# Optimization experiments

Measured on AMD Instinct MI355X. Metric: run time of the kernel, lower is better.

Reference implementation:

```python
import jax, jax.numpy as jnp
import numpy as np

LN_EPS = 1e-5

def layernorm(x, w, b):
    mu = jnp.mean(x, axis=-1, keepdims=True)
    var = jnp.mean(jnp.square(x - mu), axis=-1, keepdims=True)
    return (x - mu) * jax.lax.rsqrt(var + LN_EPS) * w + b

def l2_normalize(x, eps=1e-12):
    n = jnp.sqrt(jnp.sum(jnp.square(x), axis=-1, keepdims=True))
    return x / jnp.maximum(n, eps)

def setup_inputs() -> dict:
    key = jax.random.key(0)
    k1, k2 = jax.random.split(key)
    B, D, Npix = 8, 64, 32768
    K, P = 19, 5
    return {
        "base_feature": jax.random.normal(k1, (B, D, Npix), dtype=jnp.float32),
        "means": jax.random.normal(k2, (K, P, D), dtype=jnp.float32) * 0.02,  # trunc_normal_(std=0.02)
        "diagonal": jnp.ones((K, P, D), dtype=jnp.float32),
        "feat_w": jnp.ones((D,), dtype=jnp.float32),
        "feat_b": jnp.zeros((D,), dtype=jnp.float32),
        "mask_w": jnp.ones((K,), dtype=jnp.float32),
        "mask_b": jnp.zeros((K,), dtype=jnp.float32),
    }

def gmm_log_prob(x, mu, scale):
    # x: [N, D]; mu, scale: [KP, D]  (MultivariateNormalDiag with scale_diag=scale)
    # log p = -0.5 * sum(((x-mu)/s)^2) - sum(log s) - 0.5*D*log(2*pi)
    D = x.shape[-1]
    inv2 = 1.0 / jnp.square(scale)                      # [KP, D]
    quad = (jnp.square(x) @ inv2.T                       # [N, KP]
            - 2.0 * (x @ (mu * inv2).T)
            + jnp.sum(jnp.square(mu) * inv2, axis=-1))
    log_norm = jnp.sum(jnp.log(scale), axis=-1) + 0.5 * D * jnp.log(2.0 * jnp.pi)
    return -0.5 * quad - log_norm                        # [N, KP]

def reference(base_feature, means, diagonal, feat_w, feat_b, mask_w, mask_b):
    B, D, Npix = base_feature.shape
    K, P, _ = means.shape
    # 'b c n -> (b n) c'
    _c = jnp.transpose(base_feature, (0, 2, 1)).reshape(B * Npix, D)
    _c = layernorm(_c, feat_w, feat_b)
    _c = l2_normalize(_c)
    means_n = l2_normalize(means)                        # means.data.copy_(l2_normalize(means))
    logp = gmm_log_prob(_c, means_n.reshape(K * P, D), diagonal.reshape(K * P, D))
    final_probs = logp.reshape(-1, K, P)                 # [(b n), K, P]
    _m_prob = jnp.max(final_probs, axis=-1)              # amax over components -> [(b n), K]
    out_seg = layernorm(_m_prob, mask_w, mask_b)         # mask_norm
    # '(b n) k -> b k n'
    out_seg = jnp.transpose(out_seg.reshape(B, Npix, K), (0, 2, 1))
    return out_seg
```

## Files before the change

kernel.cpp:

```cpp
#include <hip/hip_runtime.h>
#include <math.h>

#define BB    8
#define DD    64
#define NPIX  32768
#define KK    19
#define PP    5
#define KP    95
#define KPAD  96

typedef _Float16 half8  __attribute__((ext_vector_type(8)));
typedef __fp16   half2t __attribute__((ext_vector_type(2)));
typedef float    f32x4  __attribute__((ext_vector_type(4)));

union H8 { half8 v; half2t p[4]; };

__global__ __launch_bounds__(64) void gmm_prep(
        const float* __restrict__ means, const float* __restrict__ diag,
        const float* __restrict__ feat_w, const float* __restrict__ feat_b,
        _Float16* __restrict__ Ch, float* __restrict__ cst,
        float* __restrict__ scal) {
    int j = blockIdx.x;
    int d = threadIdx.x;
    if (j < KP) {
        float mu = means[j * DD + d];
        float sc = diag[j * DD + d];
        float ss = mu * mu;
        #pragma unroll
        for (int off = 32; off; off >>= 1) ss += __shfl_xor(ss, off);
        float inv = 1.f / fmaxf(sqrtf(ss), 1e-12f);
        float mn = mu * inv;
        float i2 = 1.f / (sc * sc);
        Ch[j * 128 + 2 * d]     = (_Float16)(mn * i2);
        Ch[j * 128 + 2 * d + 1] = (_Float16)(-0.5f * i2);
        float c1 = mn * mn * i2;
        float c2 = logf(sc);
        #pragma unroll
        for (int off = 32; off; off >>= 1) {
            c1 += __shfl_xor(c1, off);
            c2 += __shfl_xor(c2, off);
        }
        if (d == 0) cst[j] = -0.5f * c1 - c2 - 58.8120661251f;
    } else {
        Ch[95 * 128 + 2 * d]     = (_Float16)0.f;
        Ch[95 * 128 + 2 * d + 1] = (_Float16)0.f;
        float w = feat_w[d], b = feat_b[d];
        float s0 = w * w, s1 = w * b, s2 = b * b;
        #pragma unroll
        for (int off = 32; off; off >>= 1) {
            s0 += __shfl_xor(s0, off);
            s1 += __shfl_xor(s1, off);
            s2 += __shfl_xor(s2, off);
        }
        if (d == 0) { cst[95] = 0.f; scal[0] = s0; scal[1] = s1; scal[2] = s2; }
    }
}

#define LPS 98

__global__ __launch_bounds__(256, 2) void gmm_main(
        const float* __restrict__ bf,
        const float* __restrict__ feat_w, const float* __restrict__ feat_b,
        const float* __restrict__ mask_w, const float* __restrict__ mask_b,
        const _Float16* __restrict__ Ch, const float* __restrict__ cst,
        const float* __restrict__ scal, float* __restrict__ out) {
    __shared__ float lds[4][32 * LPS];

    const int tid  = threadIdx.x;
    const int w    = tid >> 6;
    const int lane = tid & 63;
    const int m15  = lane & 15;
    const int q    = lane >> 4;
    const int bidx = blockIdx.x;
    const int b    = bidx >> 8;
    const int n0   = ((bidx & 255) << 7) + (w << 5);
    float* lp = lds[w];

    const float* xp = bf + (size_t)b * (DD * NPIX) + n0 + m15;
    float xs0[16], xs1[16];
    #pragma unroll
    for (int ks = 0; ks < 4; ++ks)
        #pragma unroll
        for (int i = 0; i < 4; ++i) {
            const size_t off = (size_t)(ks * 16 + q * 4 + i) * NPIX;
            xs0[ks * 4 + i] = xp[off];
            xs1[ks * 4 + i] = xp[off + 16];
        }

    float4 wv[4], bv[4];
    #pragma unroll
    for (int ks = 0; ks < 4; ++ks) {
        wv[ks] = *(const float4*)(feat_w + ks * 16 + q * 4);
        bv[ks] = *(const float4*)(feat_b + ks * 16 + q * 4);
    }

    float S1a = 0.f, S2a = 0.f, S3a = 0.f, S4a = 0.f, S5a = 0.f;
    float S1b = 0.f, S2b = 0.f, S3b = 0.f, S4b = 0.f, S5b = 0.f;
    #pragma unroll
    for (int ks = 0; ks < 4; ++ks)
        #pragma unroll
        for (int i = 0; i < 4; ++i) {
            float wd = ((const float*)&wv[ks])[i];
            float bd = ((const float*)&bv[ks])[i];
            float xa = xs0[ks * 4 + i], xb = xs1[ks * 4 + i];
            float ta = wd * xa, tb = wd * xb;
            S1a += xa; S2a = fmaf(xa, xa, S2a); S3a = fmaf(ta, ta, S3a);
            S4a = fmaf(ta, wd, S4a); S5a = fmaf(ta, bd, S5a);
            S1b += xb; S2b = fmaf(xb, xb, S2b); S3b = fmaf(tb, tb, S3b);
            S4b = fmaf(tb, wd, S4b); S5b = fmaf(tb, bd, S5b);
        }
    S1a += __shfl_xor(S1a, 16); S1a += __shfl_xor(S1a, 32);
    S2a += __shfl_xor(S2a, 16); S2a += __shfl_xor(S2a, 32);
    S3a += __shfl_xor(S3a, 16); S3a += __shfl_xor(S3a, 32);
    S4a += __shfl_xor(S4a, 16); S4a += __shfl_xor(S4a, 32);
    S5a += __shfl_xor(S5a, 16); S5a += __shfl_xor(S5a, 32);
    S1b += __shfl_xor(S1b, 16); S1b += __shfl_xor(S1b, 32);
    S2b += __shfl_xor(S2b, 16); S2b += __shfl_xor(S2b, 32);
    S3b += __shfl_xor(S3b, 16); S3b += __shfl_xor(S3b, 32);
    S4b += __shfl_xor(S4b, 16); S4b += __shfl_xor(S4b, 32);
    S5b += __shfl_xor(S5b, 16); S5b += __shfl_xor(S5b, 32);

    const float W2 = scal[0], WB = scal[1], B2 = scal[2];
    float al0, e0, f0, al1, e1, f1;
    {
        float mu  = S1a * (1.f / 64.f);
        float var = fmaxf(S2a * (1.f / 64.f) - mu * mu, 0.f);
        float r   = rsqrtf(var + 1e-5f);
        float Sy2 = r * r * (S3a - 2.f * mu * S4a + mu * mu * W2)
                  + 2.f * r * (S5a - mu * WB) + B2;
        float invn = 1.f / fmaxf(sqrtf(fmaxf(Sy2, 0.f)), 1e-12f);
        al0 = invn * r; e0 = invn; f0 = -al0 * mu;
    }
    {
        float mu  = S1b * (1.f / 64.f);
        float var = fmaxf(S2b * (1.f / 64.f) - mu * mu, 0.f);
        float r   = rsqrtf(var + 1e-5f);
        float Sy2 = r * r * (S3b - 2.f * mu * S4b + mu * mu * W2)
                  + 2.f * r * (S5b - mu * WB) + B2;
        float invn = 1.f / fmaxf(sqrtf(fmaxf(Sy2, 0.f)), 1e-12f);
        al1 = invn * r; e1 = invn; f1 = -al1 * mu;
    }

    H8 Uh[2][4], Ul[2][4];
    #pragma unroll
    for (int ks = 0; ks < 4; ++ks) {
        #pragma unroll
        for (int i = 0; i < 4; ++i) {
            float wd = ((const float*)&wv[ks])[i];
            float bd = ((const float*)&bv[ks])[i];
            float c0 = fmaf(f0, wd, e0 * bd);
            float c1 = fmaf(f1, wd, e1 * bd);
            float u0 = fmaf(al0, wd * xs0[ks * 4 + i], c0);
            float u1 = fmaf(al1, wd * xs1[ks * 4 + i], c1);
            float q0 = u0 * u0, q1 = u1 * u1;
            half2t h0 = __builtin_amdgcn_cvt_pkrtz(u0, q0);
            half2t h1 = __builtin_amdgcn_cvt_pkrtz(u1, q1);
            half2t l0 = __builtin_amdgcn_cvt_pkrtz(u0 - (float)h0[0], q0 - (float)h0[1]);
            half2t l1 = __builtin_amdgcn_cvt_pkrtz(u1 - (float)h1[0], q1 - (float)h1[1]);
            Uh[0][ks].p[i] = h0; Ul[0][ks].p[i] = l0;
            Uh[1][ks].p[i] = h1; Ul[1][ks].p[i] = l1;
        }
    }

    const _Float16* cb = Ch + (size_t)m15 * 128 + q * 8;
    half8 Ac[4];
    #pragma unroll
    for (int ks = 0; ks < 4; ++ks) Ac[ks] = *(const half8*)(cb + ks * 32);
    float4 cc = *(const float4*)(cst + 4 * q);

    #pragma unroll 2
    for (int t = 0; t < 6; ++t) {
        half8 An[4];
        float4 cn;
        if (t < 5) {
            const _Float16* nb = cb + (size_t)(16 * (t + 1)) * 128;
            #pragma unroll
            for (int ks = 0; ks < 4; ++ks) An[ks] = *(const half8*)(nb + ks * 32);
            cn = *(const float4*)(cst + 16 * (t + 1) + 4 * q);
        }
        f32x4 a0 = {0.f, 0.f, 0.f, 0.f}, a1 = a0;
        #pragma unroll
        for (int ks = 0; ks < 4; ++ks) {
            a0 = __builtin_amdgcn_mfma_f32_16x16x32_f16(Ac[ks], Uh[0][ks].v, a0, 0, 0, 0);
            a1 = __builtin_amdgcn_mfma_f32_16x16x32_f16(Ac[ks], Uh[1][ks].v, a1, 0, 0, 0);
        }
        #pragma unroll
        for (int ks = 0; ks < 4; ++ks) {
            a0 = __builtin_amdgcn_mfma_f32_16x16x32_f16(Ac[ks], Ul[0][ks].v, a0, 0, 0, 0);
            a1 = __builtin_amdgcn_mfma_f32_16x16x32_f16(Ac[ks], Ul[1][ks].v, a1, 0, 0, 0);
        }
        {
            const int j0 = 16 * t + 4 * q;
            float2 v00 = make_float2(a0[0] + cc[0], a0[1] + cc[1]);
            float2 v01 = make_float2(a0[2] + cc[2], a0[3] + cc[3]);
            float2 v10 = make_float2(a1[0] + cc[0], a1[1] + cc[1]);
            float2 v11 = make_float2(a1[2] + cc[2], a1[3] + cc[3]);
            *(float2*)(lp + m15 * LPS + j0)            = v00;
            *(float2*)(lp + m15 * LPS + j0 + 2)        = v01;
            *(float2*)(lp + (16 + m15) * LPS + j0)     = v10;
            *(float2*)(lp + (16 + m15) * LPS + j0 + 2) = v11;
        }
        if (t < 5) {
            #pragma unroll
            for (int ks = 0; ks < 4; ++ks) Ac[ks] = An[ks];
            cc = cn;
        }
    }

    const int px2 = lane & 31;
    const int h   = lane >> 5;
    const int kb  = h ? 9 : 0;
    const int ke  = h ? 19 : 9;
    const float* rowp = lp + px2 * LPS;
    float mv[10];
    float S = 0.f;
    #pragma unroll
    for (int kk = 0; kk < 10; ++kk) {
        const int k = kb + kk;
        float best = -3.4e38f;
        if (k < ke) {
            #pragma unroll
            for (int p = 0; p < PP; ++p)
                best = fmaxf(best, rowp[5 * k + p]);
            S += best;
        }
        mv[kk] = best;
    }
    S += __shfl_xor(S, 32);
    const float mum = S * (1.f / 19.f);
    float V = 0.f;
    #pragma unroll
    for (int kk = 0; kk < 10; ++kk) {
        if (kb + kk < ke) { float t = mv[kk] - mum; V = fmaf(t, t, V); }
    }
    V += __shfl_xor(V, 32);
    const float rm = rsqrtf(V * (1.f / 19.f) + 1e-5f);

    float* op = out + (size_t)b * (KK * NPIX) + n0 + px2;
    #pragma unroll
    for (int kk = 0; kk < 10; ++kk) {
        const int k = kb + kk;
        if (k < ke)
            op[(size_t)k * NPIX] = (mv[kk] - mum) * rm * mask_w[k] + mask_b[k];
    }
}

extern "C" void kernel_launch(void* const* d_in, const int* in_sizes, int n_in,
                              void* d_out, int out_size, void* d_ws, size_t ws_size,
                              hipStream_t stream) {
    const float* base_feature = (const float*)d_in[0];
    const float* means        = (const float*)d_in[1];
    const float* diagonal     = (const float*)d_in[2];
    const float* feat_w       = (const float*)d_in[3];
    const float* feat_b       = (const float*)d_in[4];
    const float* mask_w       = (const float*)d_in[5];
    const float* mask_b       = (const float*)d_in[6];
    float* out = (float*)d_out;

    _Float16* Ch = (_Float16*)d_ws;
    float* cst   = (float*)(Ch + KPAD * 128);
    float* scal  = cst + KPAD;

    gmm_prep<<<KPAD, 64, 0, stream>>>(means, diagonal, feat_w, feat_b, Ch, cst, scal);

    gmm_main<<<(BB * NPIX) / 128, 256, 0, stream>>>(
        base_feature, feat_w, feat_b, mask_w, mask_b, Ch, cst, scal, out);
}
```

Baseline: 137.9 us.

## Permute GMM component rows so max and mask-norm stay in MFMA registers

The prep kernel reorders the component rows (padded to 112) so that each MFMA output lane holds the same component index for a fixed cluster across tiles. The max over components, the mask layernorm and the output then run directly on accumulator registers with cross-lane shuffles, which removes the LDS staging buffer and the shared-memory round trip. Dropping the LDS lets the launch bounds rise to 4 blocks per SM, but the kernel now runs 7 MFMA tiles instead of 6, which is extra padded compute. The constant log-normalisation term is dropped because the final layernorm cancels it.

Result: slower. 140.8 us (+2.1%).

```diff
diff --git a/kernel.cpp b/kernel.cpp
--- a/kernel.cpp
+++ b/kernel.cpp
@@ -6,8 +6,7 @@
 #define NPIX  32768
 #define KK    19
 #define PP    5
-#define KP    95
-#define KPAD  96
+#define NROW  112
 
 typedef _Float16 half8  __attribute__((ext_vector_type(8)));
 typedef __fp16   half2t __attribute__((ext_vector_type(2)));
@@ -20,9 +19,26 @@
         const float* __restrict__ feat_w, const float* __restrict__ feat_b,
         _Float16* __restrict__ Ch, float* __restrict__ cst,
         float* __restrict__ scal) {
-    int j = blockIdx.x;
-    int d = threadIdx.x;
-    if (j < KP) {
+    const int R = blockIdx.x;
+    const int d = threadIdx.x;
+    if (R == NROW) {
+        float w = feat_w[d], b = feat_b[d];
+        float s0 = w * w, s1 = w * b, s2 = b * b;
+        #pragma unroll
+        for (int off = 32; off; off >>= 1) {
+            s0 += __shfl_xor(s0, off);
+            s1 += __shfl_xor(s1, off);
+            s2 += __shfl_xor(s2, off);
+        }
+        if (d == 0) { scal[0] = s0; scal[1] = s1; scal[2] = s2; }
+        return;
+    }
+    int g, p; bool valid;
+    if (R < 80)      { g = 4 * (R >> 4) + ((R >> 2) & 3); p = R & 3; valid = (g < KK); }
+    else if (R < 96) { g = 4 * ((R - 80) & 3) + ((R - 80) >> 2); p = 4; valid = true; }
+    else             { g = 16 + ((R - 96) >> 2); p = 4; valid = ((R & 3) == 0) && (g < KK); }
+    if (valid) {
+        const int j = 5 * g + p;
         float mu = means[j * DD + d];
         float sc = diag[j * DD + d];
         float ss = mu * mu;
@@ -31,8 +47,8 @@
         float inv = 1.f / fmaxf(sqrtf(ss), 1e-12f);
         float mn = mu * inv;
         float i2 = 1.f / (sc * sc);
-        Ch[j * 128 + 2 * d]     = (_Float16)(mn * i2);
-        Ch[j * 128 + 2 * d + 1] = (_Float16)(-0.5f * i2);
+        Ch[R * 128 + 2 * d]     = (_Float16)(mn * i2);
+        Ch[R * 128 + 2 * d + 1] = (_Float16)(-0.5f * i2);
         float c1 = mn * mn * i2;
         float c2 = logf(sc);
         #pragma unroll
@@ -40,32 +56,65 @@
             c1 += __shfl_xor(c1, off);
             c2 += __shfl_xor(c2, off);
         }
-        if (d == 0) cst[j] = -0.5f * c1 - c2 - 58.8120661251f;
+        if (d == 0) cst[R] = -0.5f * c1 - c2;
     } else {
-        Ch[95 * 128 + 2 * d]     = (_Float16)0.f;
-        Ch[95 * 128 + 2 * d + 1] = (_Float16)0.f;
-        float w = feat_w[d], b = feat_b[d];
-        float s0 = w * w, s1 = w * b, s2 = b * b;
-        #pragma unroll
-        for (int off = 32; off; off >>= 1) {
-            s0 += __shfl_xor(s0, off);
-            s1 += __shfl_xor(s1, off);
-            s2 += __shfl_xor(s2, off);
-        }
-        if (d == 0) { cst[95] = 0.f; scal[0] = s0; scal[1] = s1; scal[2] = s2; }
-    }
-}
-
-#define LPS 98
-
-__global__ __launch_bounds__(256, 2) void gmm_main(
+        Ch[R * 128 + 2 * d]     = (_Float16)0.f;
+        Ch[R * 128 + 2 * d + 1] = (_Float16)0.f;
+        if (d == 0) cst[R] = 0.f;
+    }
+}
+
+#define DO_TILE(T, MERGE) {                                                   \
+    const _Float16* ab = cb + (size_t)((T) * 16 * 128);                       \
+    const half8 A0 = *(const half8*)(ab);                                     \
+    const half8 A1 = *(const half8*)(ab + 32);                                \
+    const half8 A2 = *(const half8*)(ab + 64);                                \
+    const half8 A3 = *(const half8*)(ab + 96);                                \
+    const float4 cc = *(const float4*)(cst + 16 * (T) + 4 * q);               \
+    f32x4 a0 = {0.f, 0.f, 0.f, 0.f}, a1 = {0.f, 0.f, 0.f, 0.f};               \
+    a0 = __builtin_amdgcn_mfma_f32_16x16x32_f16(A0, Uh[0][0].v, a0, 0, 0, 0); \
+    a1 = __builtin_amdgcn_mfma_f32_16x16x32_f16(A0, Uh[1][0].v, a1, 0, 0, 0); \
+    a0 = __builtin_amdgcn_mfma_f32_16x16x32_f16(A1, Uh[0][1].v, a0, 0, 0, 0); \
+    a1 = __builtin_amdgcn_mfma_f32_16x16x32_f16(A1, Uh[1][1].v, a1, 0, 0, 0); \
+    a0 = __builtin_amdgcn_mfma_f32_16x16x32_f16(A2, Uh[0][2].v, a0, 0, 0, 0); \
+    a1 = __builtin_amdgcn_mfma_f32_16x16x32_f16(A2, Uh[1][2].v, a1, 0, 0, 0); \
+    a0 = __builtin_amdgcn_mfma_f32_16x16x32_f16(A3, Uh[0][3].v, a0, 0, 0, 0); \
+    a1 = __builtin_amdgcn_mfma_f32_16x16x32_f16(A3, Uh[1][3].v, a1, 0, 0, 0); \
+    a0 = __builtin_amdgcn_mfma_f32_16x16x32_f16(A0, Ul[0][0].v, a0, 0, 0, 0); \
+    a1 = __builtin_amdgcn_mfma_f32_16x16x32_f16(A0, Ul[1][0].v, a1, 0, 0, 0); \
+    a0 = __builtin_amdgcn_mfma_f32_16x16x32_f16(A1, Ul[0][1].v, a0, 0, 0, 0); \
+    a1 = __builtin_amdgcn_mfma_f32_16x16x32_f16(A1, Ul[1][1].v, a1, 0, 0, 0); \
+    a0 = __builtin_amdgcn_mfma_f32_16x16x32_f16(A2, Ul[0][2].v, a0, 0, 0, 0); \
+    a1 = __builtin_amdgcn_mfma_f32_16x16x32_f16(A2, Ul[1][2].v, a1, 0, 0, 0); \
+    a0 = __builtin_amdgcn_mfma_f32_16x16x32_f16(A3, Ul[0][3].v, a0, 0, 0, 0); \
+    a1 = __builtin_amdgcn_mfma_f32_16x16x32_f16(A3, Ul[1][3].v, a1, 0, 0, 0); \
+    MERGE                                                                     \
+}
+
+#define MERGE_SLOT(T)                                                              \
+    m0[T] = fmaxf(fmaxf(a0[0] + cc.x, a0[1] + cc.y), fmaxf(a0[2] + cc.z, a0[3] + cc.w)); \
+    m1[T] = fmaxf(fmaxf(a1[0] + cc.x, a1[1] + cc.y), fmaxf(a1[2] + cc.z, a1[3] + cc.w));
+
+#define MERGE_C4A                                                \
+    m0[0] = fmaxf(m0[0], a0[0] + cc.x);                          \
+    m0[1] = fmaxf(m0[1], a0[1] + cc.y);                          \
+    m0[2] = fmaxf(m0[2], a0[2] + cc.z);                          \
+    m0[3] = fmaxf(m0[3], a0[3] + cc.w);                          \
+    m1[0] = fmaxf(m1[0], a1[0] + cc.x);                          \
+    m1[1] = fmaxf(m1[1], a1[1] + cc.y);                          \
+    m1[2] = fmaxf(m1[2], a1[2] + cc.z);                          \
+    m1[3] = fmaxf(m1[3], a1[3] + cc.w);
+
+#define MERGE_C4B                                                \
+    m0[4] = fmaxf(m0[4], a0[0] + cc.x);                          \
+    m1[4] = fmaxf(m1[4], a1[0] + cc.x);
+
+__global__ __launch_bounds__(256, 4) void gmm_main(
         const float* __restrict__ bf,
         const float* __restrict__ feat_w, const float* __restrict__ feat_b,
         const float* __restrict__ mask_w, const float* __restrict__ mask_b,
         const _Float16* __restrict__ Ch, const float* __restrict__ cst,
         const float* __restrict__ scal, float* __restrict__ out) {
-    __shared__ float lds[4][32 * LPS];
-
     const int tid  = threadIdx.x;
     const int w    = tid >> 6;
     const int lane = tid & 63;
@@ -74,7 +123,6 @@
     const int bidx = blockIdx.x;
     const int b    = bidx >> 8;
     const int n0   = ((bidx & 255) << 7) + (w << 5);
-    float* lp = lds[w];
 
     const float* xp = bf + (size_t)b * (DD * NPIX) + n0 + m15;
     float xs0[16], xs1[16];
@@ -163,85 +211,46 @@
     }
 
     const _Float16* cb = Ch + (size_t)m15 * 128 + q * 8;
-    half8 Ac[4];
-    #pragma unroll
-    for (int ks = 0; ks < 4; ++ks) Ac[ks] = *(const half8*)(cb + ks * 32);
-    float4 cc = *(const float4*)(cst + 4 * q);
-
-    #pragma unroll 2
-    for (int t = 0; t < 6; ++t) {
-        half8 An[4];
-        float4 cn;
-        if (t < 5) {
-            const _Float16* nb = cb + (size_t)(16 * (t + 1)) * 128;
-            #pragma unroll
-            for (int ks = 0; ks < 4; ++ks) An[ks] = *(const half8*)(nb + ks * 32);
-            cn = *(const float4*)(cst + 16 * (t + 1) + 4 * q);
-        }
-        f32x4 a0 = {0.f, 0.f, 0.f, 0.f}, a1 = a0;
-        #pragma unroll
-        for (int ks = 0; ks < 4; ++ks) {
-            a0 = __builtin_amdgcn_mfma_f32_16x16x32_f16(Ac[ks], Uh[0][ks].v, a0, 0, 0, 0);
-            a1 = __builtin_amdgcn_mfma_f32_16x16x32_f16(Ac[ks], Uh[1][ks].v, a1, 0, 0, 0);
-        }
-        #pragma unroll
-        for (int ks = 0; ks < 4; ++ks) {
-            a0 = __builtin_amdgcn_mfma_f32_16x16x32_f16(Ac[ks], Ul[0][ks].v, a0, 0, 0, 0);
-            a1 = __builtin_amdgcn_mfma_f32_16x16x32_f16(Ac[ks], Ul[1][ks].v, a1, 0, 0, 0);
-        }
-        {
-            const int j0 = 16 * t + 4 * q;
-            float2 v00 = make_float2(a0[0] + cc[0], a0[1] + cc[1]);
-            float2 v01 = make_float2(a0[2] + cc[2], a0[3] + cc[3]);
-            float2 v10 = make_float2(a1[0] + cc[0], a1[1] + cc[1]);
-            float2 v11 = make_float2(a1[2] + cc[2], a1[3] + cc[3]);
-            *(float2*)(lp + m15 * LPS + j0)            = v00;
-            *(float2*)(lp + m15 * LPS + j0 + 2)        = v01;
-            *(float2*)(lp + (16 + m15) * LPS + j0)     = v10;
-            *(float2*)(lp + (16 + m15) * LPS + j0 + 2) = v11;
-        }
-        if (t < 5) {
-            #pragma unroll
-            for (int ks = 0; ks < 4; ++ks) Ac[ks] = An[ks];
-            cc = cn;
-        }
-    }
-
-    const int px2 = lane & 31;
-    const int h   = lane >> 5;
-    const int kb  = h ? 9 : 0;
-    const int ke  = h ? 19 : 9;
-    const float* rowp = lp + px2 * LPS;
-    float mv[10];
-    float S = 0.f;
-    #pragma unroll
-    for (int kk = 0; kk < 10; ++kk) {
-        const int k = kb + kk;
-        float best = -3.4e38f;
-        if (k < ke) {
-            #pragma unroll
-            for (int p = 0; p < PP; ++p)
-                best = fmaxf(best, rowp[5 * k + p]);
-            S += best;
-        }
-        mv[kk] = best;
-    }
-    S += __shfl_xor(S, 32);
-    const float mum = S * (1.f / 19.f);
-    float V = 0.f;
-    #pragma unroll
-    for (int kk = 0; kk < 10; ++kk) {
-        if (kb + kk < ke) { float t = mv[kk] - mum; V = fmaf(t, t, V); }
-    }
-    V += __shfl_xor(V, 32);
-    const float rm = rsqrtf(V * (1.f / 19.f) + 1e-5f);
-
-    float* op = out + (size_t)b * (KK * NPIX) + n0 + px2;
-    #pragma unroll
-    for (int kk = 0; kk < 10; ++kk) {
-        const int k = kb + kk;
-        if (k < ke)
-            op[(size_t)k * NPIX] = (mv[kk] - mum) * rm * mask_w[k] + mask_b[k];
+    float m0[5], m1[5];
+    DO_TILE(0, MERGE_SLOT(0))
+    DO_TILE(1, MERGE_SLOT(1))
+    DO_TILE(2, MERGE_SLOT(2))
+    DO_TILE(3, MERGE_SLOT(3))
+    DO_TILE(4, MERGE_SLOT(4))
+    DO_TILE(5, MERGE_C4A)
+    DO_TILE(6, MERGE_C4B)
+
+    const bool v4 = (q < 3);
+    float S0 = m0[0] + m0[1] + m0[2] + m0[3] + (v4 ? m0[4] : 0.f);
+    float S1 = m1[0] + m1[1] + m1[2] + m1[3] + (v4 ? m1[4] : 0.f);
+    S0 += __shfl_xor(S0, 16); S0 += __shfl_xor(S0, 32);
+    S1 += __shfl_xor(S1, 16); S1 += __shfl_xor(S1, 32);
+    const float mu0 = S0 * (1.f / 19.f), mu1 = S1 * (1.f / 19.f);
+    float V0, V1;
+    {
+        float d0 = m0[0] - mu0, d1 = m0[1] - mu0, d2 = m0[2] - mu0;
+        float d3 = m0[3] - mu0, d4 = m0[4] - mu0;
+        V0 = d0 * d0 + d1 * d1 + d2 * d2 + d3 * d3 + (v4 ? d4 * d4 : 0.f);
+    }
+    {
+        float d0 = m1[0] - mu1, d1 = m1[1] - mu1, d2 = m1[2] - mu1;
+        float d3 = m1[3] - mu1, d4 = m1[4] - mu1;
+        V1 = d0 * d0 + d1 * d1 + d2 * d2 + d3 * d3 + (v4 ? d4 * d4 : 0.f);
+    }
+    V0 += __shfl_xor(V0, 16); V0 += __shfl_xor(V0, 32);
+    V1 += __shfl_xor(V1, 16); V1 += __shfl_xor(V1, 32);
+    const float r0 = rsqrtf(V0 * (1.f / 19.f) + 1e-5f);
+    const float r1 = rsqrtf(V1 * (1.f / 19.f) + 1e-5f);
+
+    float* op = out + (size_t)b * (KK * NPIX) + n0 + m15;
+    #pragma unroll
+    for (int t = 0; t < 5; ++t) {
+        const int k = 4 * t + q;
+        if (t < 4 || v4) {
+            const float mw = mask_w[k], mb = mask_b[k];
+            op[(size_t)k * NPIX]      = (m0[t] - mu0) * r0 * mw + mb;
+            op[(size_t)k * NPIX + 16] = (m1[t] - mu1) * r1 * mw + mb;
+        }
     }
 }
 
@@ -258,10 +267,10 @@
     float* out = (float*)d_out;
 
     _Float16* Ch = (_Float16*)d_ws;
-    float* cst   = (float*)(Ch + KPAD * 128);
-    float* scal  = cst + KPAD;
-
-    gmm_prep<<<KPAD, 64, 0, stream>>>(means, diagonal, feat_w, feat_b, Ch, cst, scal);
+    float* cst   = (float*)(Ch + NROW * 128);
+    float* scal  = cst + NROW;
+
+    gmm_prep<<<NROW + 1, 64, 0, stream>>>(means, diagonal, feat_w, feat_b, Ch, cst, scal);
 
     gmm_main<<<(BB * NPIX) / 128, 256, 0, stream>>>(
         base_feature, feat_w, feat_b, mask_w, mask_b, Ch, cst, scal, out);
```
